# Kernel optimization log

Hardware: AMD Instinct MI355X
Metric: run time of the kernel (lower is better)

The kernel has to match this reference:

```python
import jax, jax.numpy as jnp
import numpy as np

B, T, V, D, P, DEP = 64, 32, 32000, 1024, 8, 4
TAU = 1.0
EPS = 1e-5


def setup_inputs() -> dict:
    key = jax.random.key(0)
    ks = jax.random.split(key, 9)
    s = 0.02
    x = jax.random.randint(ks[0], (B, T), 0, V)
    emb = jax.random.normal(ks[1], (V, D), jnp.float32) * s
    pos = jax.random.normal(ks[2], (T, D), jnp.float32) * s
    # primitive library: n_prims MLPs (Linear -> GELU -> Linear), stacked
    w1 = jax.random.normal(ks[3], (P, D, D), jnp.float32) * s
    b1 = jnp.zeros((P, D), jnp.float32)
    w2 = jax.random.normal(ks[4], (P, D, D), jnp.float32) * s
    b2 = jnp.zeros((P, D), jnp.float32)
    # one selector Linear(dim, n_prims) per depth
    sel_w = jax.random.normal(ks[5], (DEP, P, D), jnp.float32) * s
    sel_b = jnp.zeros((DEP, P), jnp.float32)
    ln_g = jnp.ones((D,), jnp.float32)
    ln_b = jnp.zeros((D,), jnp.float32)
    head_w = jax.random.normal(ks[6], (V, D), jnp.float32) * s
    # fixed gumbel noise (replaces torch's in-op sampling, kept deterministic)
    u = jax.random.uniform(ks[7], (DEP, B, P), jnp.float32, 1e-6, 1.0 - 1e-6)
    gumbel = -jnp.log(-jnp.log(u))
    return dict(x=x, emb=emb, pos=pos, w1=w1, b1=b1, w2=w2, b2=b2,
                sel_w=sel_w, sel_b=sel_b, ln_g=ln_g, ln_b=ln_b,
                head_w=head_w, gumbel=gumbel)


def reference(x, emb, pos, w1, b1, w2, b2, sel_w, sel_b, ln_g, ln_b, head_w, gumbel):
    h = emb[x] + pos[None, :x.shape[1], :]          # [B,T,D]
    div = jnp.float32(0.0)
    unif = jnp.float32(1.0 / P)
    for d in range(DEP):
        ctx = h.mean(axis=1)                         # [B,D]
        logits = ctx @ sel_w[d].T + sel_b[d]         # [B,P]
        weights = jax.nn.softmax((logits + gumbel[d]) / TAU, axis=-1)
        # all primitives over all tokens at once (grouped GEMM), no T loop
        u1 = jax.nn.gelu(jnp.einsum('btd,pde->btpe', h, w1) + b1, approximate=False)
        prim = jnp.einsum('btpe,pef->btpf', u1, w2) + b2   # [B,T,P,D]
        h = h + jnp.einsum('btpf,bp->btf', prim, weights)  # residual add
        avg = weights.mean(axis=0)                   # [P]
        # F.kl_div(avg.log(), uniform, reduction='sum')
        div = div + jnp.sum(unif * (jnp.log(unif) - jnp.log(avg)))
    mu = h.mean(-1, keepdims=True)
    var = ((h - mu) ** 2).mean(-1, keepdims=True)
    hn = (h - mu) * jax.lax.rsqrt(var + EPS) * ln_g + ln_b
    return hn @ head_w.T, div
```

## Files before the change

kernel.cpp:

```cpp
#include <hip/hip_runtime.h>
#include <hip/hip_bf16.h>
#include <math.h>

typedef __bf16 bf16x8 __attribute__((ext_vector_type(8)));
typedef float  f32x4  __attribute__((ext_vector_type(4)));

struct __align__(8) bf16x4s { __hip_bfloat16 a, b, c, d; };

__device__ __forceinline__ void gload_lds16(const void* g, void* l) {
  __builtin_amdgcn_global_load_lds(
      (const __attribute__((address_space(1))) void*)g,
      (__attribute__((address_space(3))) void*)l, 16, 0, 0);
}

__device__ __forceinline__ float fast_gelu(float v) {
  float s = 0.70710678118654752f * v;
  float a = fabsf(s);
  float t = __builtin_amdgcn_rcpf(fmaf(0.3275911f, a, 1.0f));
  float p = t * fmaf(t, fmaf(t, fmaf(t, fmaf(t, 1.061405429f, -1.453152027f),
                                     1.421413741f), -0.284496736f), 0.254829592f);
  float e = __expf(-a * a);
  float er = copysignf(fmaf(-p, e, 1.0f), s);
  return 0.5f * v * (1.0f + er);
}

template<int EPI>
__global__ __launch_bounds__(512, 2)
void gemm_nt(const __hip_bfloat16* __restrict__ A,
             const __hip_bfloat16* __restrict__ B,
             const int K, const int Kc, const int N,
             const float* __restrict__ p0,
             const float* __restrict__ p1,
             float* __restrict__ f32out,
             __hip_bfloat16* __restrict__ bfout)
{
  __shared__ __align__(16) __hip_bfloat16 lds[65536];

  const int tid = threadIdx.x;
  const int lane = tid & 63, wid = tid >> 6;
  const int l15 = lane & 15, l4 = lane >> 4;
  const int r8 = lane >> 3, blk = lane & 7;
  const int wm = wid >> 2, wn = wid & 3;

  const int nx = gridDim.x;
  const int flat = blockIdx.x + nx * blockIdx.y;
  const int q = (nx * gridDim.y) >> 3;
  const int nid = (flat & 7) * q + (flat >> 3);
  const long m0 = (long)(nid % nx) * 256;
  const long n0 = (long)(nid / nx) * 256;

  const int kbeg = blockIdx.z * Kc;
  const int nt = Kc / 64;

  f32x4 acc[8][4] = {};

  auto stage = [&](int buf, int k0) {
    __hip_bfloat16* dA = lds + buf * 16384;
    __hip_bfloat16* dB = lds + 32768 + buf * 16384;
#pragma unroll
    for (int p2 = 0; p2 < 4; ++p2) {
      int ch = p2 * 8 + wid;
      int row = ch * 8 + r8;
      gload_lds16(A + (m0 + row) * (long)K + k0 + ((blk ^ r8) << 3), dA + ch * 512);
    }
#pragma unroll
    for (int p2 = 0; p2 < 4; ++p2) {
      int ch = p2 * 8 + wid;
      int row = ch * 8 + r8;
      gload_lds16(B + (n0 + row) * (long)K + k0 + ((blk ^ r8) << 3), dB + ch * 512);
    }
  };

  stage(0, kbeg);
  stage(1, kbeg + 64);
  asm volatile("s_waitcnt vmcnt(8)" ::: "memory");
  __builtin_amdgcn_sched_barrier(0);
  __builtin_amdgcn_s_barrier();

  for (int t = 0; t < nt; ++t) {
    const __hip_bfloat16* pA = lds + (t & 1) * 16384;
    const __hip_bfloat16* pB = lds + 32768 + (t & 1) * 16384;

    bf16x8 a0[4][2], bv[4][2];
#pragma unroll
    for (int mi = 0; mi < 4; ++mi)
#pragma unroll
      for (int kk = 0; kk < 2; ++kk) {
        int row = wm * 128 + mi * 16 + l15;
        a0[mi][kk] = *(const bf16x8*)(pA + row * 64 + (((kk * 4 + l4) ^ (row & 7)) << 3));
      }
#pragma unroll
    for (int nj = 0; nj < 4; ++nj)
#pragma unroll
      for (int kk = 0; kk < 2; ++kk) {
        int row = wn * 64 + nj * 16 + l15;
        bv[nj][kk] = *(const bf16x8*)(pB + row * 64 + (((kk * 4 + l4) ^ (row & 7)) << 3));
      }
    __builtin_amdgcn_s_setprio(1);
#pragma unroll
    for (int mi = 0; mi < 4; ++mi)
#pragma unroll
      for (int nj = 0; nj < 4; ++nj)
#pragma unroll
        for (int kk = 0; kk < 2; ++kk)
          acc[mi][nj] = __builtin_amdgcn_mfma_f32_16x16x32_bf16(a0[mi][kk], bv[nj][kk], acc[mi][nj], 0, 0, 0);
    __builtin_amdgcn_s_setprio(0);

    bf16x8 a1[4][2];
#pragma unroll
    for (int mi = 0; mi < 4; ++mi)
#pragma unroll
      for (int kk = 0; kk < 2; ++kk) {
        int row = wm * 128 + 64 + mi * 16 + l15;
        a1[mi][kk] = *(const bf16x8*)(pA + row * 64 + (((kk * 4 + l4) ^ (row & 7)) << 3));
      }
    asm volatile("s_waitcnt lgkmcnt(0)" ::: "memory");
    __builtin_amdgcn_sched_barrier(0);
    __builtin_amdgcn_s_barrier();

    if (t + 2 < nt) {
      stage(t & 1, kbeg + (t + 2) * 64);
      asm volatile("s_waitcnt vmcnt(8)" ::: "memory");
    } else {
      asm volatile("s_waitcnt vmcnt(0)" ::: "memory");
    }
    __builtin_amdgcn_sched_barrier(0);
    __builtin_amdgcn_s_barrier();

    __builtin_amdgcn_s_setprio(1);
#pragma unroll
    for (int mi = 0; mi < 4; ++mi)
#pragma unroll
      for (int nj = 0; nj < 4; ++nj)
#pragma unroll
        for (int kk = 0; kk < 2; ++kk)
          acc[4 + mi][nj] = __builtin_amdgcn_mfma_f32_16x16x32_bf16(a1[mi][kk], bv[nj][kk], acc[4 + mi][nj], 0, 0, 0);
    __builtin_amdgcn_s_setprio(0);
  }

  const long slab = (EPI == 2) ? (long)blockIdx.z * (long)(gridDim.x * 256) * N : 0;
#pragma unroll
  for (int mi = 0; mi < 8; ++mi) {
    const long gmb = m0 + wm * 128 + mi * 16 + l4 * 4;
    const int b = (int)(gmb >> 5);
#pragma unroll
    for (int nj = 0; nj < 4; ++nj) {
      const long gn = n0 + wn * 64 + nj * 16 + l15;
      if constexpr (EPI == 0) {
        const int p = (int)(gn >> 10), e = (int)(gn & 1023);
        const float bias = p0[(p << 10) + e];
        const float wpb = p1[(b << 3) + p];
#pragma unroll
        for (int r = 0; r < 4; ++r) {
          float v = fast_gelu(acc[mi][nj][r] + bias) * wpb;
          bfout[(gmb + r) * (long)N + gn] = __float2bfloat16(v);
        }
      } else {
#pragma unroll
        for (int r = 0; r < 4; ++r)
          f32out[slab + (gmb + r) * (long)N + gn] = acc[mi][nj][r];
      }
    }
  }
}

__global__ void cvt_bf16_k(const float* __restrict__ in, __hip_bfloat16* __restrict__ out, long n) {
  long i = ((long)blockIdx.x * blockDim.x + threadIdx.x) * 4;
  if (i >= n) return;
  float4 v = *(const float4*)(in + i);
  *(bf16x4s*)(out + i) = bf16x4s{__float2bfloat16(v.x), __float2bfloat16(v.y),
                                 __float2bfloat16(v.z), __float2bfloat16(v.w)};
}

__global__ void tconv_k(const float* __restrict__ in, __hip_bfloat16* __restrict__ out,
                        long in_bs, long out_rs, long out_bs) {
  __shared__ float tile[32][33];
  int p = blockIdx.z;
  int r0 = blockIdx.y * 32, c0 = blockIdx.x * 32;
  int tx = threadIdx.x, ty = threadIdx.y;
#pragma unroll
  for (int i = 0; i < 32; i += 8)
    tile[ty + i][tx] = in[(long)p * in_bs + (long)(r0 + ty + i) * 1024 + c0 + tx];
  __syncthreads();
#pragma unroll
  for (int i = 0; i < 32; i += 8)
    out[(long)(c0 + ty + i) * out_rs + (long)p * out_bs + (r0 + tx)] =
        __float2bfloat16(tile[tx][ty + i]);
}

__global__ void embed_k(const int* __restrict__ x, const float* __restrict__ emb,
                        const float* __restrict__ pos, float* __restrict__ h,
                        __hip_bfloat16* __restrict__ hb, float* __restrict__ divp) {
  int row = blockIdx.x;
  int t = row & 31;
  int c = threadIdx.x * 4;
  long tok = x[row];
  float4 e = *(const float4*)(emb + tok * 1024 + c);
  float4 q = *(const float4*)(pos + (long)t * 1024 + c);
  float4 v{e.x + q.x, e.y + q.y, e.z + q.z, e.w + q.w};
  *(float4*)(h + (long)row * 1024 + c) = v;
  *(bf16x4s*)(hb + (long)row * 1024 + c) =
      bf16x4s{__float2bfloat16(v.x), __float2bfloat16(v.y),
              __float2bfloat16(v.z), __float2bfloat16(v.w)};
  if (row == 0 && threadIdx.x == 0) *divp = 0.f;
}

__global__ void select_k(const float* __restrict__ h, const float* __restrict__ selw,
                         const float* __restrict__ selb, const float* __restrict__ gum,
                         float* __restrict__ W, int dep) {
  int b = blockIdx.x, tid = threadIdx.x;
  int c = tid * 4;
  float4 s{0.f, 0.f, 0.f, 0.f};
  for (int t = 0; t < 32; ++t) {
    const float4 v = *(const float4*)(h + ((long)(b * 32 + t)) * 1024 + c);
    s.x += v.x; s.y += v.y; s.z += v.z; s.w += v.w;
  }
  float lp[8];
#pragma unroll
  for (int p = 0; p < 8; ++p) {
    const float4 w = *(const float4*)(selw + dep * 8192 + p * 1024 + c);
    lp[p] = (s.x * w.x + s.y * w.y + s.z * w.z + s.w * w.w) * (1.f / 32.f);
  }
  int lane = tid & 63, wid = tid >> 6;
#pragma unroll
  for (int p = 0; p < 8; ++p)
    for (int o = 32; o; o >>= 1) lp[p] += __shfl_down(lp[p], o);
  __shared__ float red[4][8];
  if (lane == 0) {
#pragma unroll
    for (int p = 0; p < 8; ++p) red[wid][p] = lp[p];
  }
  __syncthreads();
  if (tid == 0) {
    float lg[8], mx = -1e30f;
    for (int p = 0; p < 8; ++p) {
      lg[p] = red[0][p] + red[1][p] + red[2][p] + red[3][p]
            + selb[dep * 8 + p] + gum[dep * 512 + b * 8 + p];
      mx = fmaxf(mx, lg[p]);
    }
    float sm = 0.f;
    for (int p = 0; p < 8; ++p) { lg[p] = expf(lg[p] - mx); sm += lg[p]; }
    float inv = 1.f / sm;
    for (int p = 0; p < 8; ++p) W[b * 8 + p] = lg[p] * inv;
  }
}

__global__ void wb2_k(const float* __restrict__ W, const float* __restrict__ b2,
                      float* __restrict__ wb2, float* __restrict__ divp) {
  int b = blockIdx.x;
  int c = threadIdx.x * 4;
  float4 a{0.f, 0.f, 0.f, 0.f};
#pragma unroll
  for (int p = 0; p < 8; ++p) {
    float wp = W[b * 8 + p];
    const float4 v = *(const float4*)(b2 + p * 1024 + c);
    a.x += wp * v.x; a.y += wp * v.y; a.z += wp * v.z; a.w += wp * v.w;
  }
  *(float4*)(wb2 + (long)b * 1024 + c) = a;
  if (b == 0 && threadIdx.x == 0) {
    float s[8] = {0.f, 0.f, 0.f, 0.f, 0.f, 0.f, 0.f, 0.f};
    for (int bb = 0; bb < 64; ++bb)
#pragma unroll
      for (int p = 0; p < 8; ++p) s[p] += W[bb * 8 + p];
    float d = *divp;
    const float u = 0.125f, lu = logf(0.125f);
#pragma unroll
    for (int p = 0; p < 8; ++p) d += u * (lu - logf(s[p] * (1.f / 64.f)));
    *divp = d;
  }
}

__global__ void h_update_k(const float* __restrict__ part, float* __restrict__ h,
                           const float* __restrict__ wb2, __hip_bfloat16* __restrict__ hb) {
  int row = blockIdx.x;
  int c = threadIdx.x * 4;
  long idx = (long)row * 1024 + c;
  float4 a = *(const float4*)(h + idx);
  const float4 w = *(const float4*)(wb2 + (long)(row >> 5) * 1024 + c);
  a.x += w.x; a.y += w.y; a.z += w.z; a.w += w.w;
#pragma unroll
  for (int s = 0; s < 8; ++s) {
    const float4 v = *(const float4*)(part + (long)s * 2097152 + idx);
    a.x += v.x; a.y += v.y; a.z += v.z; a.w += v.w;
  }
  *(float4*)(h + idx) = a;
  *(bf16x4s*)(hb + idx) = bf16x4s{__float2bfloat16(a.x), __float2bfloat16(a.y),
                                  __float2bfloat16(a.z), __float2bfloat16(a.w)};
}

__global__ void ln_k(const float* __restrict__ h, const float* __restrict__ g,
                     const float* __restrict__ be, __hip_bfloat16* __restrict__ hnb,
                     const float* __restrict__ divp, float* __restrict__ divout) {
  int row = blockIdx.x, tid = threadIdx.x;
  int c = tid * 4;
  const float4 v = *(const float4*)(h + (long)row * 1024 + c);
  float s = v.x + v.y + v.z + v.w;
  float q = v.x * v.x + v.y * v.y + v.z * v.z + v.w * v.w;
  for (int o = 32; o; o >>= 1) { s += __shfl_down(s, o); q += __shfl_down(q, o); }
  __shared__ float red[16];
  int lane = tid & 63, wid = tid >> 6;
  if (lane == 0) { red[wid] = s; red[8 + wid] = q; }
  __syncthreads();
  if (tid == 0) {
    float S = red[0] + red[1] + red[2] + red[3];
    float Q = red[8] + red[9] + red[10] + red[11];
    float mu = S * (1.f / 1024.f);
    float var = Q * (1.f / 1024.f) - mu * mu;
    red[0] = mu; red[1] = rsqrtf(var + 1e-5f);
  }
  __syncthreads();
  float mu = red[0], rs = red[1];
  float4 gg = *(const float4*)(g + c), bb = *(const float4*)(be + c);
  *(bf16x4s*)(hnb + (long)row * 1024 + c) =
      bf16x4s{__float2bfloat16((v.x - mu) * rs * gg.x + bb.x),
              __float2bfloat16((v.y - mu) * rs * gg.y + bb.y),
              __float2bfloat16((v.z - mu) * rs * gg.z + bb.z),
              __float2bfloat16((v.w - mu) * rs * gg.w + bb.w)};
  if (row == 0 && tid == 0) *divout = *divp;
}

extern "C" void kernel_launch(void* const* d_in, const int* in_sizes, int n_in,
                              void* d_out, int out_size, void* d_ws, size_t ws_size,
                              hipStream_t stream) {
  (void)in_sizes; (void)n_in; (void)out_size; (void)ws_size;
  const int*   x     = (const int*)  d_in[0];
  const float* emb   = (const float*)d_in[1];
  const float* pos   = (const float*)d_in[2];
  const float* w1    = (const float*)d_in[3];
  const float* b1    = (const float*)d_in[4];
  const float* w2    = (const float*)d_in[5];
  const float* b2    = (const float*)d_in[6];
  const float* selw  = (const float*)d_in[7];
  const float* selb  = (const float*)d_in[8];
  const float* lng   = (const float*)d_in[9];
  const float* lnb   = (const float*)d_in[10];
  const float* headw = (const float*)d_in[11];
  const float* gum   = (const float*)d_in[12];
  float* out = (float*)d_out;

  char* ws = (char*)d_ws;
  __hip_bfloat16* w1t   = (__hip_bfloat16*)(ws);
  __hip_bfloat16* w2t   = (__hip_bfloat16*)(ws + 16777216);
  __hip_bfloat16* headb = (__hip_bfloat16*)(ws + 33554432);
  float*          h     = (float*)(ws + 99090432);
  __hip_bfloat16* hb    = (__hip_bfloat16*)(ws + 107479040);
  __hip_bfloat16* u1    = (__hip_bfloat16*)(ws + 111673344);
  float*          W     = (float*)(ws + 145227776);
  float*          wb2   = (float*)(ws + 145229824);
  float*          divp  = (float*)(ws + 145491968);
  float*          part  = out;

  cvt_bf16_k<<<32000, 256, 0, stream>>>(headw, headb, 32768000L);
  tconv_k<<<dim3(32, 32, 8), dim3(32, 8), 0, stream>>>(w1, w1t, 1L << 20, 1024L, 1L << 20);
  tconv_k<<<dim3(32, 32, 8), dim3(32, 8), 0, stream>>>(w2, w2t, 1L << 20, 8192L, 1024L);
  embed_k<<<2048, 256, 0, stream>>>(x, emb, pos, h, hb, divp);

  for (int d = 0; d < 4; ++d) {
    select_k<<<64, 256, 0, stream>>>(h, selw, selb, gum, W, d);
    wb2_k<<<64, 256, 0, stream>>>(W, b2, wb2, divp);
    gemm_nt<0><<<dim3(8, 32), 512, 0, stream>>>(hb, w1t, 1024, 1024, 8192, b1, W, nullptr, u1);
    gemm_nt<2><<<dim3(8, 4, 8), 512, 0, stream>>>(u1, w2t, 8192, 1024, 1024, nullptr, nullptr, part, nullptr);
    h_update_k<<<2048, 256, 0, stream>>>(part, h, wb2, hb);
  }

  ln_k<<<2048, 256, 0, stream>>>(h, lng, lnb, hb, divp, out + 65536000L);
  gemm_nt<2><<<dim3(8, 125), 512, 0, stream>>>(hb, headb, 1024, 1024, 32000, nullptr, nullptr, out, nullptr);
}
```

Measured before the change: 670.4 us.

## Split GEMM main loop into four interleaved sub-phases with finer-grained staging

Restructures the bf16 MFMA GEMM main loop into four quadrant phases per K-tile, with each phase interleaving an LDS fragment read, an async global-to-LDS load of a half-tile, and 16 MFMAs. Loads for the next tiles are issued in smaller chunks spread across the iteration instead of one bulk stage, and the loop gets explicit prologue and epilogue tails. The aim is to overlap memory traffic with compute more evenly and shorten the stalls at barriers. In exchange it adds more barriers per iteration and hand-tuned vmcnt counts that must exactly match the outstanding loads.

Measured after the change: 655.8 us. 1.02x faster.

```diff
diff --git a/kernel.cpp b/kernel.cpp
--- a/kernel.cpp
+++ b/kernel.cpp
@@ -23,6 +23,14 @@
   float er = copysignf(fmaf(-p, e, 1.0f), s);
   return 0.5f * v * (1.0f + er);
 }
+
+#define BAR()   asm volatile("s_barrier" ::: "memory")
+#define LGKM0() do { asm volatile("s_waitcnt lgkmcnt(0)" ::: "memory"); \
+                     __builtin_amdgcn_sched_barrier(0); } while (0)
+#define VMC(N)  do { asm volatile("s_waitcnt vmcnt(" #N ")" ::: "memory"); \
+                     __builtin_amdgcn_sched_barrier(0); } while (0)
+#define P1()    __builtin_amdgcn_s_setprio(1)
+#define P0()    __builtin_amdgcn_s_setprio(0)
 
 template<int EPI>
 __global__ __launch_bounds__(512, 2)
@@ -53,89 +61,131 @@
   const int nt = Kc / 64;
 
   f32x4 acc[8][4] = {};
-
-  auto stage = [&](int buf, int k0) {
-    __hip_bfloat16* dA = lds + buf * 16384;
-    __hip_bfloat16* dB = lds + 32768 + buf * 16384;
-#pragma unroll
-    for (int p2 = 0; p2 < 4; ++p2) {
-      int ch = p2 * 8 + wid;
+  bf16x8 ar[4][2], br[4][2];
+
+  auto stageA = [&](int buf, int h, int k0) {
+#pragma unroll
+    for (int p2 = 0; p2 < 2; ++p2) {
+      int ch = p2 * 16 + h * 8 + wid;
       int row = ch * 8 + r8;
-      gload_lds16(A + (m0 + row) * (long)K + k0 + ((blk ^ r8) << 3), dA + ch * 512);
-    }
-#pragma unroll
-    for (int p2 = 0; p2 < 4; ++p2) {
-      int ch = p2 * 8 + wid;
-      int row = ch * 8 + r8;
-      gload_lds16(B + (n0 + row) * (long)K + k0 + ((blk ^ r8) << 3), dB + ch * 512);
+      gload_lds16(A + (m0 + row) * (long)K + k0 + ((blk ^ r8) << 3),
+                  lds + buf * 16384 + ch * 512);
     }
   };
-
-  stage(0, kbeg);
-  stage(1, kbeg + 64);
-  asm volatile("s_waitcnt vmcnt(8)" ::: "memory");
-  __builtin_amdgcn_sched_barrier(0);
-  __builtin_amdgcn_s_barrier();
-
-  for (int t = 0; t < nt; ++t) {
-    const __hip_bfloat16* pA = lds + (t & 1) * 16384;
-    const __hip_bfloat16* pB = lds + 32768 + (t & 1) * 16384;
-
-    bf16x8 a0[4][2], bv[4][2];
+  auto stageB = [&](int buf, int h, int k0) {
+#pragma unroll
+    for (int p2 = 0; p2 < 2; ++p2) {
+      int ch = (p2 * 2 + (wid >> 2)) * 8 + h * 4 + (wid & 3);
+      int row = ch * 8 + r8;
+      gload_lds16(B + (n0 + row) * (long)K + k0 + ((blk ^ r8) << 3),
+                  lds + 32768 + buf * 16384 + ch * 512);
+    }
+  };
+  auto readA = [&](const __hip_bfloat16* pA, int mih) {
 #pragma unroll
     for (int mi = 0; mi < 4; ++mi)
 #pragma unroll
       for (int kk = 0; kk < 2; ++kk) {
-        int row = wm * 128 + mi * 16 + l15;
-        a0[mi][kk] = *(const bf16x8*)(pA + row * 64 + (((kk * 4 + l4) ^ (row & 7)) << 3));
+        int row = wm * 128 + mih * 64 + mi * 16 + l15;
+        ar[mi][kk] = *(const bf16x8*)(pA + row * 64 + (((kk * 4 + l4) ^ (row & 7)) << 3));
       }
-#pragma unroll
-    for (int nj = 0; nj < 4; ++nj)
+  };
+  auto readB2 = [&](const __hip_bfloat16* pB, int njh) {
+#pragma unroll
+    for (int nj = 0; nj < 2; ++nj)
 #pragma unroll
       for (int kk = 0; kk < 2; ++kk) {
-        int row = wn * 64 + nj * 16 + l15;
-        bv[nj][kk] = *(const bf16x8*)(pB + row * 64 + (((kk * 4 + l4) ^ (row & 7)) << 3));
+        int row = wn * 64 + njh * 32 + nj * 16 + l15;
+        br[njh * 2 + nj][kk] = *(const bf16x8*)(pB + row * 64 + (((kk * 4 + l4) ^ (row & 7)) << 3));
       }
-    __builtin_amdgcn_s_setprio(1);
+  };
+  auto mfma8 = [&](int mib, int njb) {
 #pragma unroll
     for (int mi = 0; mi < 4; ++mi)
 #pragma unroll
-      for (int nj = 0; nj < 4; ++nj)
+      for (int nj = 0; nj < 2; ++nj)
 #pragma unroll
         for (int kk = 0; kk < 2; ++kk)
-          acc[mi][nj] = __builtin_amdgcn_mfma_f32_16x16x32_bf16(a0[mi][kk], bv[nj][kk], acc[mi][nj], 0, 0, 0);
-    __builtin_amdgcn_s_setprio(0);
-
-    bf16x8 a1[4][2];
-#pragma unroll
-    for (int mi = 0; mi < 4; ++mi)
-#pragma unroll
-      for (int kk = 0; kk < 2; ++kk) {
-        int row = wm * 128 + 64 + mi * 16 + l15;
-        a1[mi][kk] = *(const bf16x8*)(pA + row * 64 + (((kk * 4 + l4) ^ (row & 7)) << 3));
-      }
-    asm volatile("s_waitcnt lgkmcnt(0)" ::: "memory");
-    __builtin_amdgcn_sched_barrier(0);
-    __builtin_amdgcn_s_barrier();
-
-    if (t + 2 < nt) {
-      stage(t & 1, kbeg + (t + 2) * 64);
-      asm volatile("s_waitcnt vmcnt(8)" ::: "memory");
-    } else {
-      asm volatile("s_waitcnt vmcnt(0)" ::: "memory");
-    }
-    __builtin_amdgcn_sched_barrier(0);
-    __builtin_amdgcn_s_barrier();
-
-    __builtin_amdgcn_s_setprio(1);
-#pragma unroll
-    for (int mi = 0; mi < 4; ++mi)
-#pragma unroll
-      for (int nj = 0; nj < 4; ++nj)
-#pragma unroll
-        for (int kk = 0; kk < 2; ++kk)
-          acc[4 + mi][nj] = __builtin_amdgcn_mfma_f32_16x16x32_bf16(a1[mi][kk], bv[nj][kk], acc[4 + mi][nj], 0, 0, 0);
-    __builtin_amdgcn_s_setprio(0);
+          acc[mib + mi][njb + nj] = __builtin_amdgcn_mfma_f32_16x16x32_bf16(
+              ar[mi][kk], br[njb + nj][kk], acc[mib + mi][njb + nj], 0, 0, 0);
+  };
+
+  stageA(0, 0, kbeg);
+  stageB(0, 0, kbeg);
+  stageB(0, 1, kbeg);
+  stageA(0, 1, kbeg);
+  stageA(1, 0, kbeg + 64);
+  stageB(1, 0, kbeg + 64);
+  stageB(1, 1, kbeg + 64);
+  VMC(10);
+  BAR();
+
+  for (int s = 0; s < nt - 2; ++s) {
+    const int b = s & 1;
+    const __hip_bfloat16* pA = lds + b * 16384;
+    const __hip_bfloat16* pB = lds + 32768 + b * 16384;
+    const int k1 = kbeg + (s + 1) * 64, k2 = kbeg + (s + 2) * 64;
+    readA(pA, 0); readB2(pB, 0);
+    stageA(b ^ 1, 1, k1);
+    BAR(); LGKM0();
+    P1(); mfma8(0, 0); P0();
+    VMC(10); BAR();
+    readB2(pB, 1);
+    stageA(b, 0, k2);
+    BAR(); LGKM0();
+    P1(); mfma8(0, 2); P0();
+    VMC(10); BAR();
+    readA(pA, 1);
+    stageB(b, 0, k2);
+    BAR(); LGKM0();
+    P1(); mfma8(4, 0); P0();
+    BAR();
+    stageB(b, 1, k2);
+    BAR();
+    P1(); mfma8(4, 2); P0();
+    VMC(10); BAR();
+  }
+
+  {
+    const int b = (nt - 2) & 1;
+    const __hip_bfloat16* pA = lds + b * 16384;
+    const __hip_bfloat16* pB = lds + 32768 + b * 16384;
+    readA(pA, 0); readB2(pB, 0);
+    stageA(b ^ 1, 1, kbeg + (nt - 1) * 64);
+    BAR(); LGKM0();
+    P1(); mfma8(0, 0); P0();
+    VMC(10); BAR();
+    readB2(pB, 1);
+    BAR(); LGKM0();
+    P1(); mfma8(0, 2); P0();
+    VMC(8); BAR();
+    readA(pA, 1);
+    BAR(); LGKM0();
+    P1(); mfma8(4, 0); P0();
+    BAR();
+    BAR();
+    P1(); mfma8(4, 2); P0();
+    VMC(4); BAR();
+  }
+  {
+    const int b = (nt - 1) & 1;
+    const __hip_bfloat16* pA = lds + b * 16384;
+    const __hip_bfloat16* pB = lds + 32768 + b * 16384;
+    readA(pA, 0); readB2(pB, 0);
+    BAR(); LGKM0();
+    P1(); mfma8(0, 0); P0();
+    VMC(2); BAR();
+    readB2(pB, 1);
+    BAR(); LGKM0();
+    P1(); mfma8(0, 2); P0();
+    VMC(0); BAR();
+    readA(pA, 1);
+    BAR(); LGKM0();
+    P1(); mfma8(4, 0); P0();
+    BAR();
+    BAR();
+    P1(); mfma8(4, 2); P0();
+    BAR();
   }
 
   const long slab = (EPI == 2) ? (long)blockIdx.z * (long)(gridDim.x * 256) * N : 0;
```
